# Kernel tuning notes

Hardware: AMD Instinct MI355X
Metric: run time of the kernel (lower is better)

The kernel has to match this reference:

```python
import jax, jax.numpy as jnp
import numpy as np

B, C, H, W = 16, 512, 96, 96
K = 32


def setup_inputs() -> dict:
    key = jax.random.key(0)
    k1, k2, k3 = jax.random.split(key, 3)
    std = 1.0 / (K * C) ** 0.5
    x = jax.random.normal(k1, (B, C, H, W), dtype=jnp.float32)
    codewords = jax.random.uniform(k2, (K, C), dtype=jnp.float32, minval=-std, maxval=std)
    scale = jax.random.uniform(k3, (K,), dtype=jnp.float32, minval=-1.0, maxval=0.0)
    return {"x": x, "codewords": codewords, "scale": scale}


def reference(x, codewords, scale):
    # x: (B, C, H, W) -> (B, N, C) with N = H*W
    b, c, h, w = x.shape
    xf = x.reshape(b, c, h * w).transpose(0, 2, 1)  # (B, N, C)
    # scaled L2: scale_k * ||x_n - c_k||^2, expanded via the identity
    x2 = jnp.sum(xf * xf, axis=-1, keepdims=True)          # (B, N, 1)
    c2 = jnp.sum(codewords * codewords, axis=-1)           # (K,)
    xc = jnp.einsum('bnc,kc->bnk', xf, codewords)          # (B, N, K)
    scaled_l2 = scale * (x2 - 2.0 * xc + c2)               # (B, N, K)
    aw = jax.nn.softmax(scaled_l2, axis=2)                 # assignment weights
    # aggregate: sum_n aw_nk * (x_n - c_k) = (aw^T x)_kc - (sum_n aw_nk) c_kc
    enc = jnp.einsum('bnk,bnc->bkc', aw, xf) - jnp.sum(aw, axis=1)[..., None] * codewords
    return enc  # (B, K, C)
```

## Files before the change

kernel.cpp:

```cpp
#include <hip/hip_runtime.h>
#include <hip/hip_bf16.h>


typedef float  f32x4  __attribute__((ext_vector_type(4)));
typedef short  bf16x8 __attribute__((ext_vector_type(8)));

namespace {
constexpr int Cc  = 512;
constexpr int Nc  = 9216;
constexpr int Kc  = 32;
constexpr int TN  = 64;
constexpr int TPG = 9;
constexpr int XROW = 68;
constexpr int SKH  = 520;
constexpr int SAH  = 72;
}

static __device__ inline unsigned short f2bf(float f) {
    unsigned int u = __float_as_uint(f);
    u += 0x7fffu + ((u >> 16) & 1u);
    return (unsigned short)(u >> 16);
}
static __device__ inline unsigned int pack_bf16(float a, float b) {
    return (unsigned int)f2bf(a) | ((unsigned int)f2bf(b) << 16);
}
static __device__ inline bf16x8 u4_frag(uint4 d) {
    union { uint4 u; bf16x8 v; } cv; cv.u = d; return cv.v;
}

__launch_bounds__(256, 1)
__global__ void enc_mfma(const float* __restrict__ x,
                         const float* __restrict__ cw,
                         const float* __restrict__ scale,
                         float* __restrict__ out)
{
    __shared__ __attribute__((aligned(16))) unsigned int   x_cp[256 * XROW];
    __shared__ __attribute__((aligned(16))) unsigned short cw_lds[Kc * SKH];
    __shared__ __attribute__((aligned(16))) unsigned short aw_lds[Kc * SAH];
    __shared__ float c2p[Kc][8];
    __shared__ float c2_lds[Kc];
    __shared__ float sc_lds[Kc];
    __shared__ float awsum[Kc];

    const int tid  = threadIdx.x;
    const int w    = tid >> 6;
    const int nloc = tid & 15;
    const int g    = (tid >> 4) & 3;

    const int b   = blockIdx.x >> 4;
    const int grp = blockIdx.x & 15;
    const float* __restrict__ xb = x + (size_t)b * Cc * Nc;

    for (int i = 0; i < 64; ++i) {
        int flat = tid + 256 * i;
        cw_lds[(flat >> 9) * SKH + (flat & 511)] = f2bf(cw[flat]);
    }
    {
        int k = tid >> 3, seg = tid & 7;
        const float* r = cw + k * Cc + seg * 64;
        float s = 0.f;
        for (int c = 0; c < 64; ++c) s = fmaf(r[c], r[c], s);
        c2p[k][seg] = s;
    }
    if (tid < Kc) { sc_lds[tid] = scale[tid]; awsum[tid] = 0.f; }
    __syncthreads();
    if (tid < Kc) {
        float s = 0.f;
        #pragma unroll
        for (int j = 0; j < 8; ++j) s += c2p[tid][j];
        c2_lds[tid] = s;
    }
    __syncthreads();

    float sc8[8], c28[8];
    #pragma unroll
    for (int i = 0; i < 8; ++i) {
        int k = 16 * (i >> 2) + 4 * g + (i & 3);
        sc8[i] = sc_lds[k];
        c28[i] = c2_lds[k];
    }

    f32x4 acc2[2][8];
    #pragma unroll
    for (int t = 0; t < 2; ++t)
        #pragma unroll
        for (int ct = 0; ct < 8; ++ct) acc2[t][ct] = (f32x4)0.f;
    float awacc[8] = {0.f,0.f,0.f,0.f,0.f,0.f,0.f,0.f};

    for (int tile = 0; tile < TPG; ++tile) {
        const int n0 = (grp * TPG + tile) * TN;
        const int nw = n0 + 16 * w;

        f32x4 acc1[2];
        acc1[0] = (f32x4)0.f; acc1[1] = (f32x4)0.f;
        float x2 = 0.f;

        __syncthreads();

        #pragma unroll 4
        for (int cs = 0; cs < 16; ++cs) {
            const float* p = xb + (size_t)(cs * 32 + g * 8) * Nc + nw + nloc;
            float v[8];
            #pragma unroll
            for (int j = 0; j < 8; ++j) v[j] = p[(size_t)j * Nc];
            unsigned int pk[4];
            #pragma unroll
            for (int j2 = 0; j2 < 4; ++j2) {
                x2 = fmaf(v[2*j2],   v[2*j2],   x2);
                x2 = fmaf(v[2*j2+1], v[2*j2+1], x2);
                pk[j2] = pack_bf16(v[2*j2], v[2*j2+1]);
                x_cp[(cs * 16 + g * 4 + j2) * XROW + 16 * w + nloc] = pk[j2];
            }
            bf16x8 bfrag = u4_frag(make_uint4(pk[0], pk[1], pk[2], pk[3]));
            #pragma unroll
            for (int t = 0; t < 2; ++t) {
                uint4 a = *(const uint4*)&cw_lds[(16*t + nloc) * SKH + cs*32 + g*8];
                acc1[t] = __builtin_amdgcn_mfma_f32_16x16x32_bf16(
                              u4_frag(a), bfrag, acc1[t], 0, 0, 0);
            }
        }

        x2 += __shfl_xor(x2, 16);
        x2 += __shfl_xor(x2, 32);
        float l[8], aw[8];
        float m = -1e30f;
        #pragma unroll
        for (int i = 0; i < 8; ++i) {
            float xc = acc1[i >> 2][i & 3];
            l[i] = sc8[i] * (x2 - 2.f * xc + c28[i]);
            m = fmaxf(m, l[i]);
        }
        m = fmaxf(m, __shfl_xor(m, 16));
        m = fmaxf(m, __shfl_xor(m, 32));
        float s = 0.f;
        #pragma unroll
        for (int i = 0; i < 8; ++i) { aw[i] = __expf(l[i] - m); s += aw[i]; }
        s += __shfl_xor(s, 16);
        s += __shfl_xor(s, 32);
        const float inv = 1.f / s;
        #pragma unroll
        for (int i = 0; i < 8; ++i) {
            aw[i] *= inv;
            awacc[i] += aw[i];
            int k = 16 * (i >> 2) + 4 * g + (i & 3);
            aw_lds[k * SAH + 16 * w + nloc] = f2bf(aw[i]);
        }
        __syncthreads();

        const int sh = (nloc & 1) * 16;
        #pragma unroll
        for (int ns = 0; ns < 2; ++ns) {
            bf16x8 afr[2];
            #pragma unroll
            for (int t = 0; t < 2; ++t)
                afr[t] = u4_frag(*(const uint4*)&aw_lds[(16*t + nloc) * SAH + ns*32 + g*8]);
            #pragma unroll
            for (int ct = 0; ct < 8; ++ct) {
                const int base = (64*w + 8*ct + (nloc >> 1)) * XROW + ns*32 + g*8;
                uint4 d0 = *(const uint4*)&x_cp[base];
                uint4 d1 = *(const uint4*)&x_cp[base + 4];
                unsigned int f0 = ((d0.x >> sh) & 0xffffu) | (((d0.y >> sh) & 0xffffu) << 16);
                unsigned int f1 = ((d0.z >> sh) & 0xffffu) | (((d0.w >> sh) & 0xffffu) << 16);
                unsigned int f2 = ((d1.x >> sh) & 0xffffu) | (((d1.y >> sh) & 0xffffu) << 16);
                unsigned int f3 = ((d1.z >> sh) & 0xffffu) | (((d1.w >> sh) & 0xffffu) << 16);
                bf16x8 bfr = u4_frag(make_uint4(f0, f1, f2, f3));
                acc2[0][ct] = __builtin_amdgcn_mfma_f32_16x16x32_bf16(afr[0], bfr, acc2[0][ct], 0,0,0);
                acc2[1][ct] = __builtin_amdgcn_mfma_f32_16x16x32_bf16(afr[1], bfr, acc2[1][ct], 0,0,0);
            }
        }
    }

    #pragma unroll
    for (int i = 0; i < 8; ++i) {
        float v = awacc[i];
        v += __shfl_xor(v, 1);
        v += __shfl_xor(v, 2);
        v += __shfl_xor(v, 4);
        v += __shfl_xor(v, 8);
        awacc[i] = v;
    }
    if (nloc == 0) {
        #pragma unroll
        for (int i = 0; i < 8; ++i) {
            int k = 16 * (i >> 2) + 4 * g + (i & 3);
            atomicAdd(&awsum[k], awacc[i]);
        }
    }
    __syncthreads();

    float* ob = out + (size_t)b * Kc * Cc;
    #pragma unroll
    for (int t = 0; t < 2; ++t)
        #pragma unroll
        for (int ct = 0; ct < 8; ++ct)
            #pragma unroll
            for (int r = 0; r < 4; ++r) {
                int k = 16 * t + 4 * g + r;
                int c = 128 * w + 16 * ct + nloc;
                float val = fmaf(-awsum[k], cw[k * Cc + c], acc2[t][ct][r]);
                atomicAdd(&ob[k * Cc + c], val);
            }
}

extern "C" void kernel_launch(void* const* d_in, const int* in_sizes, int n_in,
                              void* d_out, int out_size, void* d_ws, size_t ws_size,
                              hipStream_t stream) {
    const float* x     = (const float*)d_in[0];
    const float* cwp   = (const float*)d_in[1];
    const float* scale = (const float*)d_in[2];
    float* out = (float*)d_out;

    hipMemsetAsync(out, 0, (size_t)out_size * sizeof(float), stream);
    enc_mfma<<<dim3(256), dim3(256), 0, stream>>>(x, cwp, scale, out);
}
```

Before: 447.4 us.

## Split codeword prep into separate kernel, double grid and use vectorized x loads

Moves the bf16 conversion of the codewords and the per-codeword squared norms into a small prep kernel that writes to the workspace. The main kernel no longer keeps a codeword copy in LDS and reads its MFMA operands from global memory instead. Dropping that LDS buffer allows two blocks per CU, and the grid grows from 256 to 512 blocks, with 4 or 5 tiles each. The x tile is now loaded with coalesced float4 reads and written to LDS, with x² reduced through LDS, and the bf16 lane selection uses v_perm. The intent is better occupancy, more parallelism and wider loads. The costs are an extra kernel launch, codeword fragments fetched from global/L2 inside the inner loop, and twice as many atomic adds into the output.

After: 451.3 us. About the same (+0.9%).

```diff
diff --git a/kernel.cpp b/kernel.cpp
--- a/kernel.cpp
+++ b/kernel.cpp
@@ -6,13 +6,10 @@
 typedef short  bf16x8 __attribute__((ext_vector_type(8)));
 
 namespace {
-constexpr int Cc  = 512;
-constexpr int Nc  = 9216;
-constexpr int Kc  = 32;
-constexpr int TN  = 64;
-constexpr int TPG = 9;
+constexpr int Cc   = 512;
+constexpr int Nc   = 9216;
+constexpr int Kc   = 32;
 constexpr int XROW = 68;
-constexpr int SKH  = 520;
 constexpr int SAH  = 72;
 }
 
@@ -28,54 +25,61 @@
     union { uint4 u; bf16x8 v; } cv; cv.u = d; return cv.v;
 }
 
-__launch_bounds__(256, 1)
-__global__ void enc_mfma(const float* __restrict__ x,
-                         const float* __restrict__ cw,
-                         const float* __restrict__ scale,
-                         float* __restrict__ out)
+__global__ void enc_prep(const float* __restrict__ cw,
+                         unsigned short* __restrict__ cwb,
+                         float* __restrict__ c2)
+{
+    const int k = blockIdx.x;
+    const int t = threadIdx.x;
+    float s = 0.f;
+    #pragma unroll
+    for (int h = 0; h < 2; ++h) {
+        const int c = t + 256 * h;
+        const float v = cw[k * Cc + c];
+        cwb[k * Cc + c] = f2bf(v);
+        s = fmaf(v, v, s);
+    }
+    s += __shfl_xor(s, 1);  s += __shfl_xor(s, 2);  s += __shfl_xor(s, 4);
+    s += __shfl_xor(s, 8);  s += __shfl_xor(s, 16); s += __shfl_xor(s, 32);
+    __shared__ float ps[4];
+    if ((t & 63) == 0) ps[t >> 6] = s;
+    __syncthreads();
+    if (t == 0) c2[k] = ps[0] + ps[1] + ps[2] + ps[3];
+}
+
+__launch_bounds__(256, 2)
+__global__ void enc_mfma2(const float* __restrict__ x,
+                          const float* __restrict__ cw,
+                          const float* __restrict__ scale,
+                          const unsigned short* __restrict__ cwb,
+                          const float* __restrict__ c2g,
+                          float* __restrict__ out)
 {
     __shared__ __attribute__((aligned(16))) unsigned int   x_cp[256 * XROW];
-    __shared__ __attribute__((aligned(16))) unsigned short cw_lds[Kc * SKH];
     __shared__ __attribute__((aligned(16))) unsigned short aw_lds[Kc * SAH];
-    __shared__ float c2p[Kc][8];
-    __shared__ float c2_lds[Kc];
-    __shared__ float sc_lds[Kc];
-    __shared__ float awsum[Kc];
+    __shared__ __attribute__((aligned(16))) float x2p[4][64];
+    __shared__ float sc_lds[Kc], c2_lds[Kc], awsum[Kc];
 
     const int tid  = threadIdx.x;
-    const int w    = tid >> 6;
+    const int wv   = tid >> 6;
     const int nloc = tid & 15;
     const int g    = (tid >> 4) & 3;
-
-    const int b   = blockIdx.x >> 4;
-    const int grp = blockIdx.x & 15;
+    const int i_q  = tid & 15;
+    const int cp0  = tid >> 4;
+
+    const int b   = blockIdx.x >> 5;
+    const int grp = blockIdx.x & 31;
+    const int tstart = (grp < 16) ? grp * 5 : 80 + (grp - 16) * 4;
+    const int tcnt   = (grp < 16) ? 5 : 4;
     const float* __restrict__ xb = x + (size_t)b * Cc * Nc;
 
-    for (int i = 0; i < 64; ++i) {
-        int flat = tid + 256 * i;
-        cw_lds[(flat >> 9) * SKH + (flat & 511)] = f2bf(cw[flat]);
-    }
-    {
-        int k = tid >> 3, seg = tid & 7;
-        const float* r = cw + k * Cc + seg * 64;
-        float s = 0.f;
-        for (int c = 0; c < 64; ++c) s = fmaf(r[c], r[c], s);
-        c2p[k][seg] = s;
-    }
-    if (tid < Kc) { sc_lds[tid] = scale[tid]; awsum[tid] = 0.f; }
+    if (tid < Kc) { sc_lds[tid] = scale[tid]; c2_lds[tid] = c2g[tid]; awsum[tid] = 0.f; }
     __syncthreads();
-    if (tid < Kc) {
-        float s = 0.f;
-        #pragma unroll
-        for (int j = 0; j < 8; ++j) s += c2p[tid][j];
-        c2_lds[tid] = s;
-    }
-    __syncthreads();
 
     float sc8[8], c28[8];
     #pragma unroll
     for (int i = 0; i < 8; ++i) {
-        int k = 16 * (i >> 2) + 4 * g + (i & 3);
+        const int k = 16 * (i >> 2) + 4 * g + (i & 3);
         sc8[i] = sc_lds[k];
         c28[i] = c2_lds[k];
     }
@@ -87,46 +91,64 @@
         for (int ct = 0; ct < 8; ++ct) acc2[t][ct] = (f32x4)0.f;
     float awacc[8] = {0.f,0.f,0.f,0.f,0.f,0.f,0.f,0.f};
 
-    for (int tile = 0; tile < TPG; ++tile) {
-        const int n0 = (grp * TPG + tile) * TN;
-        const int nw = n0 + 16 * w;
+    const unsigned psel = (nloc & 1) ? 0x07060302u : 0x05040100u;
+
+    for (int tt = 0; tt < tcnt; ++tt) {
+        const int n0 = (tstart + tt) * 64;
+        __syncthreads();
+
+        float x2q[4] = {0.f, 0.f, 0.f, 0.f};
+        #pragma unroll 8
+        for (int j = 0; j < 16; ++j) {
+            const int cp = cp0 + 16 * j;
+            const float* pa = xb + (size_t)(2 * cp) * Nc + n0 + 4 * i_q;
+            const float4 va = *(const float4*)pa;
+            const float4 vb = *(const float4*)(pa + Nc);
+            x2q[0] = fmaf(va.x, va.x, fmaf(vb.x, vb.x, x2q[0]));
+            x2q[1] = fmaf(va.y, va.y, fmaf(vb.y, vb.y, x2q[1]));
+            x2q[2] = fmaf(va.z, va.z, fmaf(vb.z, vb.z, x2q[2]));
+            x2q[3] = fmaf(va.w, va.w, fmaf(vb.w, vb.w, x2q[3]));
+            uint4 pk;
+            pk.x = pack_bf16(va.x, vb.x);
+            pk.y = pack_bf16(va.y, vb.y);
+            pk.z = pack_bf16(va.z, vb.z);
+            pk.w = pack_bf16(va.w, vb.w);
+            *(uint4*)&x_cp[cp * XROW + 4 * i_q] = pk;
+        }
+        #pragma unroll
+        for (int r = 0; r < 4; ++r) {
+            x2q[r] += __shfl_xor(x2q[r], 16);
+            x2q[r] += __shfl_xor(x2q[r], 32);
+        }
+        if ((tid & 63) < 16)
+            *(float4*)&x2p[wv][4 * i_q] = make_float4(x2q[0], x2q[1], x2q[2], x2q[3]);
+        __syncthreads();
 
         f32x4 acc1[2];
         acc1[0] = (f32x4)0.f; acc1[1] = (f32x4)0.f;
-        float x2 = 0.f;
-
-        __syncthreads();
-
         #pragma unroll 4
         for (int cs = 0; cs < 16; ++cs) {
-            const float* p = xb + (size_t)(cs * 32 + g * 8) * Nc + nw + nloc;
-            float v[8];
-            #pragma unroll
-            for (int j = 0; j < 8; ++j) v[j] = p[(size_t)j * Nc];
-            unsigned int pk[4];
-            #pragma unroll
-            for (int j2 = 0; j2 < 4; ++j2) {
-                x2 = fmaf(v[2*j2],   v[2*j2],   x2);
-                x2 = fmaf(v[2*j2+1], v[2*j2+1], x2);
-                pk[j2] = pack_bf16(v[2*j2], v[2*j2+1]);
-                x_cp[(cs * 16 + g * 4 + j2) * XROW + 16 * w + nloc] = pk[j2];
+            const int rb = (cs * 16 + g * 4) * XROW + 16 * wv + nloc;
+            uint4 bf;
+            bf.x = x_cp[rb];
+            bf.y = x_cp[rb + XROW];
+            bf.z = x_cp[rb + 2 * XROW];
+            bf.w = x_cp[rb + 3 * XROW];
+            const bf16x8 bfr = u4_frag(bf);
+            #pragma unroll
+            for (int t = 0; t < 2; ++t) {
+                const uint4 af = *(const uint4*)&cwb[(16 * t + nloc) * Cc + cs * 32 + g * 8];
+                acc1[t] = __builtin_amdgcn_mfma_f32_16x16x32_bf16(u4_frag(af), bfr, acc1[t], 0, 0, 0);
             }
-            bf16x8 bfrag = u4_frag(make_uint4(pk[0], pk[1], pk[2], pk[3]));
-            #pragma unroll
-            for (int t = 0; t < 2; ++t) {
-                uint4 a = *(const uint4*)&cw_lds[(16*t + nloc) * SKH + cs*32 + g*8];
-                acc1[t] = __builtin_amdgcn_mfma_f32_16x16x32_bf16(
-                              u4_frag(a), bfrag, acc1[t], 0, 0, 0);
-            }
-        }
-
-        x2 += __shfl_xor(x2, 16);
-        x2 += __shfl_xor(x2, 32);
+        }
+
+        const int ncol = 16 * wv + nloc;
+        const float x2 = x2p[0][ncol] + x2p[1][ncol] + x2p[2][ncol] + x2p[3][ncol];
         float l[8], aw[8];
         float m = -1e30f;
         #pragma unroll
         for (int i = 0; i < 8; ++i) {
-            float xc = acc1[i >> 2][i & 3];
+            const float xc = acc1[i >> 2][i & 3];
             l[i] = sc8[i] * (x2 - 2.f * xc + c28[i]);
             m = fmaxf(m, l[i]);
         }
@@ -142,30 +164,30 @@
         for (int i = 0; i < 8; ++i) {
             aw[i] *= inv;
             awacc[i] += aw[i];
-            int k = 16 * (i >> 2) + 4 * g + (i & 3);
-            aw_lds[k * SAH + 16 * w + nloc] = f2bf(aw[i]);
+            const int k = 16 * (i >> 2) + 4 * g + (i & 3);
+            aw_lds[k * SAH + ncol] = f2bf(aw[i]);
         }
         __syncthreads();
 
-        const int sh = (nloc & 1) * 16;
         #pragma unroll
         for (int ns = 0; ns < 2; ++ns) {
             bf16x8 afr[2];
             #pragma unroll
             for (int t = 0; t < 2; ++t)
-                afr[t] = u4_frag(*(const uint4*)&aw_lds[(16*t + nloc) * SAH + ns*32 + g*8]);
+                afr[t] = u4_frag(*(const uint4*)&aw_lds[(16 * t + nloc) * SAH + ns * 32 + g * 8]);
             #pragma unroll
             for (int ct = 0; ct < 8; ++ct) {
-                const int base = (64*w + 8*ct + (nloc >> 1)) * XROW + ns*32 + g*8;
-                uint4 d0 = *(const uint4*)&x_cp[base];
-                uint4 d1 = *(const uint4*)&x_cp[base + 4];
-                unsigned int f0 = ((d0.x >> sh) & 0xffffu) | (((d0.y >> sh) & 0xffffu) << 16);
-                unsigned int f1 = ((d0.z >> sh) & 0xffffu) | (((d0.w >> sh) & 0xffffu) << 16);
-                unsigned int f2 = ((d1.x >> sh) & 0xffffu) | (((d1.y >> sh) & 0xffffu) << 16);
-                unsigned int f3 = ((d1.z >> sh) & 0xffffu) | (((d1.w >> sh) & 0xffffu) << 16);
-                bf16x8 bfr = u4_frag(make_uint4(f0, f1, f2, f3));
-                acc2[0][ct] = __builtin_amdgcn_mfma_f32_16x16x32_bf16(afr[0], bfr, acc2[0][ct], 0,0,0);
-                acc2[1][ct] = __builtin_amdgcn_mfma_f32_16x16x32_bf16(afr[1], bfr, acc2[1][ct], 0,0,0);
+                const int base = (64 * wv + 8 * ct + (nloc >> 1)) * XROW + ns * 32 + g * 8;
+                const uint4 d0 = *(const uint4*)&x_cp[base];
+                const uint4 d1 = *(const uint4*)&x_cp[base + 4];
+                uint4 fb;
+                fb.x = __builtin_amdgcn_perm(d0.y, d0.x, psel);
+                fb.y = __builtin_amdgcn_perm(d0.w, d0.z, psel);
+                fb.z = __builtin_amdgcn_perm(d1.y, d1.x, psel);
+                fb.w = __builtin_amdgcn_perm(d1.w, d1.z, psel);
+                const bf16x8 bfr = u4_frag(fb);
+                acc2[0][ct] = __builtin_amdgcn_mfma_f32_16x16x32_bf16(afr[0], bfr, acc2[0][ct], 0, 0, 0);
+                acc2[1][ct] = __builtin_amdgcn_mfma_f32_16x16x32_bf16(afr[1], bfr, acc2[1][ct], 0, 0, 0);
             }
         }
     }
@@ -182,7 +204,7 @@
     if (nloc == 0) {
         #pragma unroll
         for (int i = 0; i < 8; ++i) {
-            int k = 16 * (i >> 2) + 4 * g + (i & 3);
+            const int k = 16 * (i >> 2) + 4 * g + (i & 3);
             atomicAdd(&awsum[k], awacc[i]);
         }
     }
@@ -195,9 +217,9 @@
         for (int ct = 0; ct < 8; ++ct)
             #pragma unroll
             for (int r = 0; r < 4; ++r) {
-                int k = 16 * t + 4 * g + r;
-                int c = 128 * w + 16 * ct + nloc;
-                float val = fmaf(-awsum[k], cw[k * Cc + c], acc2[t][ct][r]);
+                const int k = 16 * t + 4 * g + r;
+                const int c = 128 * wv + 16 * ct + nloc;
+                const float val = fmaf(-awsum[k], cw[k * Cc + c], acc2[t][ct][r]);
                 atomicAdd(&ob[k * Cc + c], val);
             }
 }
@@ -210,6 +232,10 @@
     const float* scale = (const float*)d_in[2];
     float* out = (float*)d_out;
 
+    unsigned short* cwb = (unsigned short*)d_ws;
+    float*          c2  = (float*)((char*)d_ws + Kc * Cc * sizeof(unsigned short));
+
     hipMemsetAsync(out, 0, (size_t)out_size * sizeof(float), stream);
-    enc_mfma<<<dim3(256), dim3(256), 0, stream>>>(x, cwp, scale, out);
-}
+    enc_prep<<<dim3(Kc), dim3(256), 0, stream>>>(cwp, cwb, c2);
+    enc_mfma2<<<dim3(512), dim3(256), 0, stream>>>(x, cwp, scale, cwb, c2, out);
+}
```
